# Optimization experiments

Hardware: AMD Instinct MI355X
Metric: run time of the kernel (lower is better)

## Reference

```python
import jax, jax.numpy as jnp
import numpy as np

# Mamba2 defaults with d_model=512, headdim=2*d_model (=> nheads=1)
D_MODEL = 512
D_INNER = 2 * D_MODEL          # expand=2
D_STATE = 128
NHEADS = 1                     # d_inner // headdim = 1
HEADDIM = D_INNER              # headdim = 2*hidden_dim
D_CONV = 4
NG = 1                         # ngroups
EPS = 1e-5


def setup_inputs() -> dict:
    key = jax.random.key(0)
    ks = jax.random.split(key, 8)
    B, L = 4, 2048
    d_in_proj = 2 * D_INNER + 2 * NG * D_STATE + NHEADS   # 2305
    conv_ch = D_INNER + 2 * NG * D_STATE                  # 1280
    x = jax.random.normal(ks[0], (B, L, D_MODEL), jnp.float32)
    rnn_state = jax.random.normal(ks[1], (B, D_MODEL), jnp.float32)
    W_in = jax.random.normal(ks[2], (d_in_proj, D_MODEL), jnp.float32) * (D_MODEL ** -0.5)
    conv_w = jax.random.normal(ks[3], (conv_ch, 1, D_CONV), jnp.float32) * (D_CONV ** -0.5)
    conv_b = jnp.zeros((conv_ch,), jnp.float32)
    # dt_bias = inv_softplus(dt) with dt ~ U(1e-3, 0.1), as in Mamba2 init
    dt = jax.random.uniform(ks[4], (NHEADS,), jnp.float32, 1e-3, 0.1)
    dt_bias = jnp.log(jnp.expm1(dt))
    A_log = jnp.log(jax.random.uniform(ks[5], (NHEADS,), jnp.float32, 1.0, 16.0))
    Dp = jnp.ones((NHEADS,), jnp.float32)
    norm_w = jnp.ones((D_INNER,), jnp.float32)
    W_out = jax.random.normal(ks[6], (D_MODEL, D_INNER), jnp.float32) * (D_INNER ** -0.5)
    return dict(x=x, rnn_state=rnn_state, W_in=W_in, conv_w=conv_w, conv_b=conv_b,
                dt_bias=dt_bias, A_log=A_log, Dp=Dp, norm_w=norm_w, W_out=W_out)


def _mamba2(x, W_in, conv_w, conv_b, dt_bias, A_log, Dp, norm_w, W_out):
    B, L, _ = x.shape
    zxbcdt = jnp.einsum('bld,ed->ble', x, W_in)           # (B,L,2305)
    z, xBC, dt = jnp.split(zxbcdt, [D_INNER, 2 * D_INNER + 2 * NG * D_STATE], axis=-1)
    # causal depthwise conv1d over channels (B,C,L), then silu
    xBC = xBC.transpose(0, 2, 1)
    xBC = jax.lax.conv_general_dilated(
        xBC, conv_w, window_strides=(1,), padding=[(D_CONV - 1, 0)],
        feature_group_count=xBC.shape[1], dimension_numbers=('NCH', 'OIH', 'NCH'))
    xBC = jax.nn.silu(xBC + conv_b[None, :, None]).transpose(0, 2, 1)
    xs, Bm, Cm = jnp.split(xBC, [D_INNER, D_INNER + NG * D_STATE], axis=-1)
    xs = xs.reshape(B, L, NHEADS, HEADDIM)
    dt = jax.nn.softplus(dt + dt_bias)                    # (B,L,H)
    A = -jnp.exp(A_log)                                   # (H,)
    dA = jnp.exp(dt * A)                                  # (B,L,H)

    # selective state-space scan: h_t = dA_t*h_{t-1} + dt_t * x_t (x) B_t ; y_t = h_t @ C_t
    def step(state, inp):
        x_t, dt_t, dA_t, B_t, C_t = inp
        state = dA_t[:, :, None, None] * state \
            + (dt_t[:, :, None] * x_t)[..., None] * B_t[:, None, None, :]
        y_t = jnp.einsum('bhpn,bn->bhp', state, C_t)
        return state, y_t

    init = jnp.zeros((B, NHEADS, HEADDIM, D_STATE), x.dtype)
    inputs = (xs.transpose(1, 0, 2, 3), dt.transpose(1, 0, 2), dA.transpose(1, 0, 2),
              Bm.transpose(1, 0, 2), Cm.transpose(1, 0, 2))
    _, ys = jax.lax.scan(step, init, inputs)              # (L,B,H,P)
    y = ys.transpose(1, 0, 2, 3) + Dp[None, None, :, None] * xs
    y = y.reshape(B, L, D_INNER)
    # gated RMSNorm (gate first, norm_before_gate=False)
    y = y * jax.nn.silu(z)
    y = y * jax.lax.rsqrt(jnp.mean(y * y, axis=-1, keepdims=True) + EPS) * norm_w
    return jnp.einsum('bld,od->blo', y, W_out)


def reference(x, rnn_state, W_in, conv_w, conv_b, dt_bias, A_log, Dp, norm_w, W_out):
    out = _mamba2(x, W_in, conv_w, conv_b, dt_bias, A_log, Dp, norm_w, W_out)
    return (out, rnn_state)
```

## Files before the change

### kernel.cpp

```cpp
#include <hip/hip_runtime.h>
#include <cstdint>
#include <cstddef>


typedef __bf16 bf16_t;
typedef __bf16 bf16x8 __attribute__((ext_vector_type(8)));
typedef __bf16 bf16x4 __attribute__((ext_vector_type(4)));
typedef __bf16 bf16x2 __attribute__((ext_vector_type(2)));
typedef float  f32x4  __attribute__((ext_vector_type(4)));

#define BATCH   4
#define SEQLEN  2048
#define MROWS   8192
#define DMODEL  512
#define DINNER  1024
#define DSTATE  128
#define NZX     2304
#define NCONV   1280
#define CHUNK   128
#define NCHUNK  16
#define NBC     64

__device__ __forceinline__ float siluf(float x) { return x / (1.f + __expf(-x)); }

__device__ __forceinline__ void load_lds16(const bf16_t* g, bf16_t* l)
{
    __builtin_amdgcn_global_load_lds(
        (const __attribute__((address_space(1))) void*)g,
        (__attribute__((address_space(3))) void*)l,
        16, 0, 0);
}

template <typename OutT>
__device__ __forceinline__ void gemm64_body(
    unsigned char* smem,
    const bf16_t* __restrict__ A, const bf16_t* __restrict__ B,
    OutT* __restrict__ C, int Ntot, int K, int lda, int ldb, int bn, int bm)
{
    bf16_t* As = (bf16_t*)smem;
    bf16_t* Bs = (bf16_t*)(smem + 8192);

    const int tid  = threadIdx.x;
    const int wave = tid >> 6, lane = tid & 63;
    const int lr = lane & 15, q = lane >> 4;
    const int wm = (wave & 1) * 32, wn = (wave >> 1) * 64;

    f32x4 acc[2][4];
    #pragma unroll
    for (int i = 0; i < 2; ++i)
        #pragma unroll
        for (int j = 0; j < 4; ++j)
            acc[i][j] = (f32x4){0.f, 0.f, 0.f, 0.f};

    const int row_a0 = bm * 64, row_b0 = bn * 128;
    const int srow = tid >> 3;
    const int gsw  = (((tid & 7) ^ (srow & 7))) * 8;
    const int lsl  = (tid & 7) * 8;

    for (int kt = 0; kt < K; kt += 64) {
        #pragma unroll
        for (int i = 0; i < 2; ++i) {
            int row = srow + i * 32;
            load_lds16(&A[(size_t)(row_a0 + row) * lda + kt + gsw], &As[row * 64 + lsl]);
        }
        #pragma unroll
        for (int i = 0; i < 4; ++i) {
            int row = srow + i * 32;
            load_lds16(&B[(size_t)(row_b0 + row) * ldb + kt + gsw], &Bs[row * 64 + lsl]);
        }
        __syncthreads();
        #pragma unroll
        for (int k0 = 0; k0 < 64; k0 += 32) {
            bf16x8 af[2], bfr[4];
            #pragma unroll
            for (int mi = 0; mi < 2; ++mi) {
                int r = wm + mi * 16 + lr, kc = (k0 >> 3) + q;
                af[mi] = *reinterpret_cast<const bf16x8*>(
                    &As[r * 64 + ((kc ^ (r & 7)) << 3)]);
            }
            #pragma unroll
            for (int ni = 0; ni < 4; ++ni) {
                int r = wn + ni * 16 + lr, kc = (k0 >> 3) + q;
                bfr[ni] = *reinterpret_cast<const bf16x8*>(
                    &Bs[r * 64 + ((kc ^ (r & 7)) << 3)]);
            }
            #pragma unroll
            for (int mi = 0; mi < 2; ++mi)
                #pragma unroll
                for (int ni = 0; ni < 4; ++ni)
                    acc[mi][ni] = __builtin_amdgcn_mfma_f32_16x16x32_bf16(
                        af[mi], bfr[ni], acc[mi][ni], 0, 0, 0);
        }
        __syncthreads();
    }

    #pragma unroll
    for (int mi = 0; mi < 2; ++mi)
        #pragma unroll
        for (int ni = 0; ni < 4; ++ni)
            #pragma unroll
            for (int ri = 0; ri < 4; ++ri) {
                int row = row_a0 + wm + mi * 16 + q * 4 + ri;
                int col = row_b0 + wn + ni * 16 + lr;
                C[(size_t)row * Ntot + col] = (OutT)acc[mi][ni][ri];
            }
}

__device__ __forceinline__ void cumsum_body(
    const float* __restrict__ dtv, const float* __restrict__ A_log,
    float* __restrict__ sarr, float* __restrict__ Pv,
    float* __restrict__ EdTv, float* __restrict__ chp, int bc)
{
    __shared__ float w0sum, stot;
    int j = threadIdx.x;
    bool active = j < CHUNK;
    int lane = j & 63;
    int r = bc * CHUNK + j;
    float A = -expf(A_log[0]);
    float dt = active ? dtv[r] : 0.f;
    float s = dt;
    #pragma unroll
    for (int m = 1; m <= 32; m <<= 1) {
        float o = __shfl_up(s, m);
        if (lane >= m) s += o;
    }
    if (j == 63) w0sum = s;
    __syncthreads();
    if (j >= 64 && active) s += w0sum;
    if (j == 127) stot = s;
    __syncthreads();
    if (active) {
        float sT = stot;
        sarr[r] = s;
        Pv[r]   = expf(A * s);
        EdTv[r] = expf(A * (sT - s)) * dt;
        if (j == 127) chp[bc] = expf(A * sT);
    }
}

__global__ __launch_bounds__(256) void gemm1_kernel(
    const bf16_t* __restrict__ xb, const bf16_t* __restrict__ winb,
    bf16_t* __restrict__ zx, const float* __restrict__ dtv,
    const float* __restrict__ A_log, float* __restrict__ sarr,
    float* __restrict__ Pv, float* __restrict__ EdTv, float* __restrict__ chp)
{
    __shared__ __align__(16) unsigned char smem[24576];
    int linear = blockIdx.x;
    if (linear < (NZX / 128) * (MROWS / 64)) {
        int xcd = linear & 7, j = linear >> 3;
        int bm = xcd * 16 + (j & 15);
        int bn = j >> 4;
        gemm64_body<bf16_t>(smem, xb, winb, zx, NZX, DMODEL, DMODEL, DMODEL, bn, bm);
    } else {
        cumsum_body(dtv, A_log, sarr, Pv, EdTv, chp, linear - 2304);
    }
}

__global__ __launch_bounds__(256) void gemm2_kernel(
    const bf16_t* __restrict__ yb, const bf16_t* __restrict__ woutb,
    float* __restrict__ out)
{
    __shared__ __align__(16) unsigned char smem[24576];
    int id  = blockIdx.x;
    int xcd = id & 7, j = id >> 3;
    int bm  = xcd * 16 + (j & 15);
    int bn  = j >> 4;
    gemm64_body<float>(smem, yb, woutb, out, DMODEL, DINNER, DINNER, DINNER, bn, bm);
}

__device__ __forceinline__ void mbuild_body(
    unsigned char* smem,
    const float* __restrict__ sarr, const float* __restrict__ dtv,
    const float* __restrict__ Pv, const float* __restrict__ A_log,
    const bf16_t* __restrict__ xbc, bf16_t* __restrict__ Mx, int bc)
{
    bf16_t* Cs  = (bf16_t*)smem;
    bf16_t* Bs2 = (bf16_t*)(smem + 32768);
    float* sj = (float*)(smem + 65536);
    float* dj = (float*)(smem + 65536 + 512);
    float* pj = (float*)(smem + 65536 + 1024);

    int tid = threadIdx.x;
    if (tid < CHUNK) {
        sj[tid] = sarr[bc * CHUNK + tid];
        dj[tid] = dtv[bc * CHUNK + tid];
        pj[tid] = Pv[bc * CHUNK + tid];
    }
    int rowbase = bc * 128;
    int srow = tid >> 4;
    int gsw  = (((tid & 15) ^ (srow & 7))) * 8;
    int lsl  = (tid & 15) * 8;
    #pragma unroll
    for (int i = 0; i < 8; ++i) {
        int row = srow + i * 16;
        load_lds16(&xbc[(size_t)(rowbase + row) * NCONV + 1152 + gsw], &Cs[row * 128 + lsl]);
        load_lds16(&xbc[(size_t)(rowbase + row) * NCONV + 1024 + gsw], &Bs2[row * 128 + lsl]);
    }
    __syncthreads();

    const int wave = tid >> 6, lane = tid & 63;
    const int lr = lane & 15, q = lane >> 4;
    const int wm = (wave & 1) * 64, wn = (wave >> 1) * 64;

    f32x4 acc[4][4];
    #pragma unroll
    for (int i = 0; i < 4; ++i)
        #pragma unroll
        for (int j = 0; j < 4; ++j)
            acc[i][j] = (f32x4){0.f, 0.f, 0.f, 0.f};

    #pragma unroll
    for (int k0 = 0; k0 < 128; k0 += 32) {
        bf16x8 af[4], bfr[4];
        #pragma unroll
        for (int mi = 0; mi < 4; ++mi) {
            int r = wm + mi * 16 + lr, kc = (k0 >> 3) + q;
            af[mi] = *reinterpret_cast<const bf16x8*>(
                &Cs[r * 128 + ((kc ^ (r & 7)) << 3)]);
        }
        #pragma unroll
        for (int ni = 0; ni < 4; ++ni) {
            int r = wn + ni * 16 + lr, kc = (k0 >> 3) + q;
            bfr[ni] = *reinterpret_cast<const bf16x8*>(
                &Bs2[r * 128 + ((kc ^ (r & 7)) << 3)]);
        }
        #pragma unroll
        for (int mi = 0; mi < 4; ++mi)
            #pragma unroll
            for (int ni = 0; ni < 4; ++ni)
                acc[mi][ni] = __builtin_amdgcn_mfma_f32_16x16x32_bf16(
                    af[mi], bfr[ni], acc[mi][ni], 0, 0, 0);
    }

    float A = -expf(A_log[0]);
    bf16_t* MxB = Mx + (size_t)bc * 32768;
    #pragma unroll
    for (int mi = 0; mi < 4; ++mi)
        #pragma unroll
        for (int ni = 0; ni < 4; ++ni)
            #pragma unroll
            for (int ri = 0; ri < 4; ++ri) {
                int row = wm + mi * 16 + q * 4 + ri;
                int col = wn + ni * 16 + lr;
                float val = 0.f;
                if (col <= row)
                    val = acc[mi][ni][ri] * expf(A * (sj[row] - sj[col])) * dj[col];
                MxB[(size_t)row * 256 + col] = (bf16_t)val;
            }

    int rr = tid >> 1, cb2 = (tid & 1) * 64;
    float Pi = pj[rr];
    #pragma unroll
    for (int m0 = 0; m0 < 64; m0 += 8) {
        int kc = (cb2 + m0) >> 3;
        bf16x8 cv = *reinterpret_cast<const bf16x8*>(
            &Cs[rr * 128 + ((kc ^ (rr & 7)) << 3)]);
        bf16x8 o;
        #pragma unroll
        for (int m = 0; m < 8; ++m) o[m] = (bf16_t)((float)cv[m] * Pi);
        *reinterpret_cast<bf16x8*>(&MxB[(size_t)rr * 256 + 128 + cb2 + m0]) = o;
    }
}

__global__ __launch_bounds__(256) void gemmA_mbuild_kernel(
    const bf16_t* __restrict__ Xt, const bf16_t* __restrict__ Bwt,
    bf16_t* __restrict__ cstate,
    const float* __restrict__ sarr, const float* __restrict__ dtv,
    const float* __restrict__ Pv, const float* __restrict__ A_log,
    const bf16_t* __restrict__ xbc, bf16_t* __restrict__ Mx)
{
    __shared__ __align__(16) unsigned char smem[67072];
    int id = blockIdx.x;
    if (id < 1024) {
        int bc = id & 63, bm = id >> 6;
        gemm64_body<bf16_t>(smem,
            Xt + (size_t)bc * 131072, Bwt + (size_t)bc * 16384,
            cstate + (size_t)bc * 131072,
            DSTATE, CHUNK, CHUNK, CHUNK, 0, bm);
    } else {
        mbuild_body(smem, sarr, dtv, Pv, A_log, xbc, Mx, id - 1024);
    }
}

__global__ __launch_bounds__(256) void gemm_y_kernel(
    const bf16_t* __restrict__ Mx, const bf16_t* __restrict__ Xt,
    const bf16_t* __restrict__ Stb, bf16_t* __restrict__ yf)
{
    __shared__ __align__(16) bf16_t As[64 * 64];
    __shared__ __align__(16) bf16_t Bs[128 * 64];

    int id = blockIdx.x;
    int bc = id & 63;
    int t  = id >> 6;
    int half = t & 1, bn = t >> 1;

    const bf16_t* Ab = Mx  + (size_t)bc * 32768 + (size_t)half * 64 * 256;
    const bf16_t* Xb = Xt  + (size_t)bc * 131072 + (size_t)bn * 128 * 128;
    const bf16_t* Sb = Stb + (size_t)bc * 131072 + (size_t)bn * 128 * 128;
    bf16_t* Cb = yf + (size_t)bc * 131072 + (size_t)half * 64 * 1024;

    const int tid  = threadIdx.x;
    const int wave = tid >> 6, lane = tid & 63;
    const int lr = lane & 15, q = lane >> 4;
    const int wm = (wave & 1) * 32, wn = (wave >> 1) * 64;

    f32x4 acc[2][4];
    #pragma unroll
    for (int i = 0; i < 2; ++i)
        #pragma unroll
        for (int j = 0; j < 4; ++j)
            acc[i][j] = (f32x4){0.f, 0.f, 0.f, 0.f};

    const int srow = tid >> 3;
    const int gsw  = (((tid & 7) ^ (srow & 7))) * 8;
    const int lsl  = (tid & 7) * 8;

    for (int kt = 0; kt < 256; kt += 64) {
        const bf16_t* bsrc = (kt < 128) ? (Xb + kt) : (Sb + (kt - 128));
        #pragma unroll
        for (int i = 0; i < 2; ++i) {
            int row = srow + i * 32;
            load_lds16(&Ab[(size_t)row * 256 + kt + gsw], &As[row * 64 + lsl]);
        }
        #pragma unroll
        for (int i = 0; i < 4; ++i) {
            int row = srow + i * 32;
            load_lds16(&bsrc[(size_t)row * 128 + gsw], &Bs[row * 64 + lsl]);
        }
        __syncthreads();
        #pragma unroll
        for (int k0 = 0; k0 < 64; k0 += 32) {
            bf16x8 af[2], bfr[4];
            #pragma unroll
            for (int mi = 0; mi < 2; ++mi) {
                int r = wm + mi * 16 + lr, kc = (k0 >> 3) + q;
                af[mi] = *reinterpret_cast<const bf16x8*>(
                    &As[r * 64 + ((kc ^ (r & 7)) << 3)]);
            }
            #pragma unroll
            for (int ni = 0; ni < 4; ++ni) {
                int r = wn + ni * 16 + lr, kc = (k0 >> 3) + q;
                bfr[ni] = *reinterpret_cast<const bf16x8*>(
                    &Bs[r * 64 + ((kc ^ (r & 7)) << 3)]);
            }
            #pragma unroll
            for (int mi = 0; mi < 2; ++mi)
                #pragma unroll
                for (int ni = 0; ni < 4; ++ni)
                    acc[mi][ni] = __builtin_amdgcn_mfma_f32_16x16x32_bf16(
                        af[mi], bfr[ni], acc[mi][ni], 0, 0, 0);
        }
        __syncthreads();
    }

    #pragma unroll
    for (int mi = 0; mi < 2; ++mi)
        #pragma unroll
        for (int ni = 0; ni < 4; ++ni)
            #pragma unroll
            for (int ri = 0; ri < 4; ++ri) {
                int row = wm + mi * 16 + q * 4 + ri;
                int col = bn * 128 + wn + ni * 16 + lr;
                Cb[(size_t)row * 1024 + col] = (bf16_t)acc[mi][ni][ri];
            }
}

__global__ __launch_bounds__(256) void dtcast_kernel(
    const float* __restrict__ x, const float* __restrict__ W_in,
    const float* __restrict__ dt_bias, const float* __restrict__ W_out,
    float* __restrict__ dtv, bf16_t* __restrict__ xb,
    bf16_t* __restrict__ winb, bf16_t* __restrict__ woutb)
{
    int bid = blockIdx.x;
    if (bid < MROWS / 4) {
        int wave = threadIdx.x >> 6, lane = threadIdx.x & 63;
        int r = bid * 4 + wave;
        const float* xr = x + (size_t)r * DMODEL + lane * 8;
        const float* wr = W_in + (size_t)NZX * DMODEL + lane * 8;
        float4 a0 = *reinterpret_cast<const float4*>(xr);
        float4 a1 = *reinterpret_cast<const float4*>(xr + 4);
        float4 b0 = *reinterpret_cast<const float4*>(wr);
        float4 b1 = *reinterpret_cast<const float4*>(wr + 4);

        bf16x8 xo;
        xo[0] = (bf16_t)a0.x; xo[1] = (bf16_t)a0.y; xo[2] = (bf16_t)a0.z; xo[3] = (bf16_t)a0.w;
        xo[4] = (bf16_t)a1.x; xo[5] = (bf16_t)a1.y; xo[6] = (bf16_t)a1.z; xo[7] = (bf16_t)a1.w;
        *reinterpret_cast<bf16x8*>(xb + (size_t)r * DMODEL + lane * 8) = xo;

        float s = a0.x * b0.x + a0.y * b0.y + a0.z * b0.z + a0.w * b0.w
                + a1.x * b1.x + a1.y * b1.y + a1.z * b1.z + a1.w * b1.w;
        #pragma unroll
        for (int m = 32; m >= 1; m >>= 1) s += __shfl_xor(s, m);
        if (lane == 0) {
            float t  = s + dt_bias[0];
            dtv[r] = (t > 20.f) ? t : log1pf(expf(t));
        }
        return;
    }
    int i = (bid - MROWS / 4) * 256 + threadIdx.x;
    const int n4a = 2305 * DMODEL / 4, n4b = DMODEL * DINNER / 4;
    const float* src; bf16_t* dst; int j;
    if (i < n4a)            { src = W_in;  dst = winb;  j = i; }
    else if (i < n4a + n4b) { src = W_out; dst = woutb; j = i - n4a; }
    else return;
    float4 v = reinterpret_cast<const float4*>(src)[j];
    bf16x4 o;
    o[0] = (bf16_t)v.x; o[1] = (bf16_t)v.y; o[2] = (bf16_t)v.z; o[3] = (bf16_t)v.w;
    reinterpret_cast<bf16x4*>(dst)[j] = o;
}

__global__ __launch_bounds__(256) void conv_tr_kernel(
    const bf16_t* __restrict__ zx, const float* __restrict__ cw,
    const float* __restrict__ cb, const float* __restrict__ EdTv,
    bf16_t* __restrict__ xbc, bf16_t* __restrict__ Xt, bf16_t* __restrict__ Bwt)
{
    constexpr int TS = 66;
    __shared__ bf16_t tile[128 * TS];
    __shared__ float cwS[64 * 4];
    __shared__ float cbS[64];

    int id  = blockIdx.x;
    int xcd = id & 7;
    int k   = id >> 3;
    int bc  = xcd * 8 + (k & 7);
    int rest = k >> 3;
    int cg   = rest >> 1;
    int half = rest & 1;
    int c0   = cg * 128 + half * 64;
    int tid  = threadIdx.x;

    if (tid < 64) {
        float4 w = *reinterpret_cast<const float4*>(cw + (size_t)(c0 + tid) * 4);
        *reinterpret_cast<float4*>(&cwS[tid * 4]) = w;
        cbS[tid] = cb[c0 + tid];
    }
    __syncthreads();

    int lrow = tid >> 3;
    int lc8  = (tid & 7) * 8;
    int g0 = bc * 128;

    #pragma unroll
    for (int pass = 0; pass < 4; ++pass) {
        int row = pass * 32 + lrow;
        int g = g0 + row;
        int l = g & (SEQLEN - 1);
        float acc[8];
        #pragma unroll
        for (int m = 0; m < 8; ++m) acc[m] = cbS[lc8 + m];
        #pragma unroll
        for (int kk = 0; kk < 4; ++kk) {
            if (l + kk >= 3) {
                bf16x8 v = *reinterpret_cast<const bf16x8*>(
                    zx + (size_t)(g + kk - 3) * NZX + DINNER + c0 + lc8);
                #pragma unroll
                for (int m = 0; m < 8; ++m)
                    acc[m] += cwS[(lc8 + m) * 4 + kk] * (float)v[m];
            }
        }
        bf16x8 o;
        #pragma unroll
        for (int m = 0; m < 8; ++m) o[m] = (bf16_t)siluf(acc[m]);
        *reinterpret_cast<bf16x8*>(xbc + (size_t)g * NCONV + c0 + lc8) = o;
        if (cg < 9) {
            #pragma unroll
            for (int jj = 0; jj < 4; ++jj) {
                bf16x2 p; p[0] = o[jj * 2]; p[1] = o[jj * 2 + 1];
                *reinterpret_cast<bf16x2*>(&tile[row * TS + lc8 + jj * 2]) = p;
            }
        }
    }
    if (cg == 9) return;
    __syncthreads();

    const bool isB = (cg == 8);
    int jo = (tid >> 4) * 8;
    int i  = tid & 15;
    float sc[8];
    #pragma unroll
    for (int m = 0; m < 8; ++m)
        sc[m] = isB ? EdTv[bc * 128 + jo + m] : 1.f;

    #pragma unroll
    for (int pass = 0; pass < 4; ++pass) {
        int oc = pass * 16 + i;
        bf16x8 o;
        #pragma unroll
        for (int m = 0; m < 8; ++m)
            o[m] = (bf16_t)((float)tile[(jo + m) * TS + oc] * sc[m]);
        bf16_t* dst = isB
            ? (Bwt + (size_t)bc * 16384 + (size_t)(c0 - 1024 + oc) * 128 + jo)
            : (Xt + (size_t)bc * 131072 + (size_t)(c0 + oc) * 128 + jo);
        *reinterpret_cast<bf16x8*>(dst) = o;
    }
}

__global__ __launch_bounds__(256) void scan_combine_kernel(
    const bf16_t* __restrict__ cstate, const float* __restrict__ chp,
    bf16_t* __restrict__ Stb)
{
    __shared__ float chS[NCHUNK];
    int idx = blockIdx.x * 256 + threadIdx.x;
    int b   = idx >> 17;
    int np  = idx & 131071;
    if (threadIdx.x < NCHUNK) chS[threadIdx.x] = chp[b * NCHUNK + threadIdx.x];
    __syncthreads();

    const bf16_t* src = cstate + ((size_t)b << 21) + np;
    bf16_t*       dst = Stb    + ((size_t)b << 21) + np;
    float t[NCHUNK];
    #pragma unroll
    for (int c = 0; c < NCHUNK; ++c) t[c] = (float)src[(size_t)c << 17];
    float v = 0.f;
    #pragma unroll
    for (int c = 0; c < NCHUNK; ++c) {
        dst[(size_t)c << 17] = (bf16_t)v;
        v = chS[c] * v + t[c];
    }
}

__global__ __launch_bounds__(256) void gate_norm_kernel(
    const bf16_t* __restrict__ yf, const bf16_t* __restrict__ zx,
    const bf16_t* __restrict__ xbc, const float* __restrict__ Dp,
    const float* __restrict__ norm_w, bf16_t* __restrict__ yb,
    const float* __restrict__ rnn, float* __restrict__ outTail)
{
    int blk = blockIdx.x, tid = threadIdx.x;
    if (blk >= MROWS / 4) {
        int i = (blk - MROWS / 4) * 256 + tid;
        if (i < BATCH * DMODEL) outTail[i] = rnn[i];
        return;
    }
    int wave = tid >> 6, lane = tid & 63;
    int r = blk * 4 + wave;
    int p0 = lane * 8, p1 = 512 + lane * 8;
    float D0 = Dp[0];

    bf16x8 y0 = *reinterpret_cast<const bf16x8*>(yf + (size_t)r * DINNER + p0);
    bf16x8 y1 = *reinterpret_cast<const bf16x8*>(yf + (size_t)r * DINNER + p1);
    bf16x8 z0 = *reinterpret_cast<const bf16x8*>(zx + (size_t)r * NZX + p0);
    bf16x8 z1 = *reinterpret_cast<const bf16x8*>(zx + (size_t)r * NZX + p1);
    bf16x8 x0 = *reinterpret_cast<const bf16x8*>(xbc + (size_t)r * NCONV + p0);
    bf16x8 x1 = *reinterpret_cast<const bf16x8*>(xbc + (size_t)r * NCONV + p1);

    float g[16];
    #pragma unroll
    for (int m = 0; m < 8; ++m) {
        g[m]     = ((float)y0[m] + D0 * (float)x0[m]) * siluf((float)z0[m]);
        g[8 + m] = ((float)y1[m] + D0 * (float)x1[m]) * siluf((float)z1[m]);
    }
    float ss = 0.f;
    #pragma unroll
    for (int m = 0; m < 16; ++m) ss += g[m] * g[m];
    #pragma unroll
    for (int m = 32; m >= 1; m >>= 1) ss += __shfl_xor(ss, m);
    float scale = rsqrtf(ss * (1.f / 1024.f) + 1e-5f);

    const float* nw = norm_w;
    float4 w0a = *reinterpret_cast<const float4*>(nw + p0);
    float4 w0b = *reinterpret_cast<const float4*>(nw + p0 + 4);
    float4 w1a = *reinterpret_cast<const float4*>(nw + p1);
    float4 w1b = *reinterpret_cast<const float4*>(nw + p1 + 4);
    float w[16] = {w0a.x, w0a.y, w0a.z, w0a.w, w0b.x, w0b.y, w0b.z, w0b.w,
                   w1a.x, w1a.y, w1a.z, w1a.w, w1b.x, w1b.y, w1b.z, w1b.w};
    bf16x8 o0, o1;
    #pragma unroll
    for (int m = 0; m < 8; ++m) {
        o0[m] = (bf16_t)(g[m] * scale * w[m]);
        o1[m] = (bf16_t)(g[8 + m] * scale * w[8 + m]);
    }
    *reinterpret_cast<bf16x8*>(yb + (size_t)r * DINNER + p0) = o0;
    *reinterpret_cast<bf16x8*>(yb + (size_t)r * DINNER + p1) = o1;
}

extern "C" void kernel_launch(void* const* d_in, const int* in_sizes, int n_in,
                              void* d_out, int out_size, void* d_ws, size_t ws_size,
                              hipStream_t stream)
{
    const float* x        = (const float*)d_in[0];
    const float* rnn      = (const float*)d_in[1];
    const float* W_in     = (const float*)d_in[2];
    const float* conv_w   = (const float*)d_in[3];
    const float* conv_b   = (const float*)d_in[4];
    const float* dt_bias  = (const float*)d_in[5];
    const float* A_log    = (const float*)d_in[6];
    const float* Dp       = (const float*)d_in[7];
    const float* norm_w   = (const float*)d_in[8];
    const float* W_out    = (const float*)d_in[9];
    float* out = (float*)d_out;

    char* ws = (char*)d_ws;
    bf16_t* xb     = (bf16_t*)(ws + 0);
    bf16_t* Mx     = (bf16_t*)(ws + 4194304);
    bf16_t* winb   = (bf16_t*)(ws + 8388608);
    bf16_t* woutb  = (bf16_t*)(ws + 10748928);
    bf16_t* zx     = (bf16_t*)(ws + 11797504);
    float*  dtv    = (float*) (ws + 49546240);
    float*  sarr   = (float*) (ws + 49579008);
    float*  Pv     = (float*) (ws + 49611776);
    float*  EdTv   = (float*) (ws + 49644544);
    float*  chp    = (float*) (ws + 49677312);
    bf16_t* xbcb   = (bf16_t*)(ws + 49677568);
    bf16_t* Xt     = (bf16_t*)(ws + 70649088);
    bf16_t* Bwt    = (bf16_t*)(ws + 87426304);
    bf16_t* cstate = (bf16_t*)(ws + 89523456);
    bf16_t* yf     = (bf16_t*)(ws + 89523456);
    bf16_t* Stb    = (bf16_t*)(ws + 106300672);
    bf16_t* yb     = (bf16_t*)(ws + 123077888);

    {
        const int n4a = 2305 * DMODEL / 4, n4b = DMODEL * DINNER / 4;
        int grid = MROWS / 4 + (n4a + n4b + 255) / 256;
        dtcast_kernel<<<grid, 256, 0, stream>>>(
            x, W_in, dt_bias, W_out, dtv, xb, winb, woutb);
    }

    gemm1_kernel<<<2304 + NBC, 256, 0, stream>>>(
        xb, winb, zx, dtv, A_log, sarr, Pv, EdTv, chp);

    conv_tr_kernel<<<1280, 256, 0, stream>>>(
        zx, conv_w, conv_b, EdTv, xbcb, Xt, Bwt);

    gemmA_mbuild_kernel<<<1088, 256, 0, stream>>>(
        Xt, Bwt, cstate, sarr, dtv, Pv, A_log, xbcb, Mx);

    scan_combine_kernel<<<BATCH * 131072 / 256, 256, 0, stream>>>(cstate, chp, Stb);

    gemm_y_kernel<<<1024, 256, 0, stream>>>(Mx, Xt, Stb, yf);

    gate_norm_kernel<<<MROWS / 4 + 8, 256, 0, stream>>>(
        yf, zx, xbcb, Dp, norm_w, yb, rnn, out + (size_t)MROWS * DMODEL);

    gemm2_kernel<<<512, 256, 0, stream>>>(yb, woutb, out);
}
```

Measured before the change: 193.6 us.

## Shrink GEMM tiles to 64x64, split mbuild into quarters, fuse it with scan

Adds a 64x64-tile GEMM body and uses it for the chunk-state GEMM, the output projection and the y GEMM, doubling their grid sizes. The intra-chunk M-matrix build is split into four 64x64 sub-blocks with less shared memory, then moved from the gemmA kernel into the scan-combine kernel. The aim is more blocks, higher occupancy and better load balance across CUs. In exchange each block reuses less data, so global and LDS traffic per FLOP rises, and the wave count per launch goes up.

```diff
diff --git a/kernel.cpp b/kernel.cpp
--- a/kernel.cpp
+++ b/kernel.cpp
@@ -106,6 +106,77 @@
             }
 }
 
+template <typename OutT>
+__device__ __forceinline__ void gemm6464_body(
+    unsigned char* smem,
+    const bf16_t* __restrict__ A, const bf16_t* __restrict__ B,
+    OutT* __restrict__ C, int Ntot, int K, int lda, int ldb, int bn, int bm)
+{
+    bf16_t* As = (bf16_t*)smem;
+    bf16_t* Bs = (bf16_t*)(smem + 8192);
+
+    const int tid  = threadIdx.x;
+    const int wave = tid >> 6, lane = tid & 63;
+    const int lr = lane & 15, q = lane >> 4;
+    const int wm = (wave & 1) * 32, wn = (wave >> 1) * 32;
+
+    f32x4 acc[2][2];
+    #pragma unroll
+    for (int i = 0; i < 2; ++i)
+        #pragma unroll
+        for (int j = 0; j < 2; ++j)
+            acc[i][j] = (f32x4){0.f, 0.f, 0.f, 0.f};
+
+    const int row_a0 = bm * 64, row_b0 = bn * 64;
+    const int srow = tid >> 3;
+    const int gsw  = (((tid & 7) ^ (srow & 7))) * 8;
+    const int lsl  = (tid & 7) * 8;
+
+    for (int kt = 0; kt < K; kt += 64) {
+        #pragma unroll
+        for (int i = 0; i < 2; ++i) {
+            int row = srow + i * 32;
+            load_lds16(&A[(size_t)(row_a0 + row) * lda + kt + gsw], &As[row * 64 + lsl]);
+            load_lds16(&B[(size_t)(row_b0 + row) * ldb + kt + gsw], &Bs[row * 64 + lsl]);
+        }
+        __syncthreads();
+        #pragma unroll
+        for (int k0 = 0; k0 < 64; k0 += 32) {
+            bf16x8 af[2], bfr[2];
+            #pragma unroll
+            for (int mi = 0; mi < 2; ++mi) {
+                int r = wm + mi * 16 + lr, kc = (k0 >> 3) + q;
+                af[mi] = *reinterpret_cast<const bf16x8*>(
+                    &As[r * 64 + ((kc ^ (r & 7)) << 3)]);
+            }
+            #pragma unroll
+            for (int ni = 0; ni < 2; ++ni) {
+                int r = wn + ni * 16 + lr, kc = (k0 >> 3) + q;
+                bfr[ni] = *reinterpret_cast<const bf16x8*>(
+                    &Bs[r * 64 + ((kc ^ (r & 7)) << 3)]);
+            }
+            #pragma unroll
+            for (int mi = 0; mi < 2; ++mi)
+                #pragma unroll
+                for (int ni = 0; ni < 2; ++ni)
+                    acc[mi][ni] = __builtin_amdgcn_mfma_f32_16x16x32_bf16(
+                        af[mi], bfr[ni], acc[mi][ni], 0, 0, 0);
+        }
+        __syncthreads();
+    }
+
+    #pragma unroll
+    for (int mi = 0; mi < 2; ++mi)
+        #pragma unroll
+        for (int ni = 0; ni < 2; ++ni)
+            #pragma unroll
+            for (int ri = 0; ri < 4; ++ri) {
+                int row = row_a0 + wm + mi * 16 + q * 4 + ri;
+                int col = row_b0 + wn + ni * 16 + lr;
+                C[(size_t)row * Ntot + col] = (OutT)acc[mi][ni][ri];
+            }
+}
+
 __device__ __forceinline__ void cumsum_body(
     const float* __restrict__ dtv, const float* __restrict__ A_log,
     float* __restrict__ sarr, float* __restrict__ Pv,
@@ -160,25 +231,44 @@
     const bf16_t* __restrict__ yb, const bf16_t* __restrict__ woutb,
     float* __restrict__ out)
 {
-    __shared__ __align__(16) unsigned char smem[24576];
+    __shared__ __align__(16) unsigned char smem[16384];
     int id  = blockIdx.x;
     int xcd = id & 7, j = id >> 3;
     int bm  = xcd * 16 + (j & 15);
     int bn  = j >> 4;
-    gemm64_body<float>(smem, yb, woutb, out, DMODEL, DINNER, DINNER, DINNER, bn, bm);
-}
-
-__device__ __forceinline__ void mbuild_body(
+    gemm6464_body<float>(smem, yb, woutb, out, DMODEL, DINNER, DINNER, DINNER, bn, bm);
+}
+
+__global__ __launch_bounds__(256) void gemmA_kernel(
+    const bf16_t* __restrict__ Xt, const bf16_t* __restrict__ Bwt,
+    bf16_t* __restrict__ cstate)
+{
+    __shared__ __align__(16) unsigned char smem[16384];
+    int id = blockIdx.x;
+    int bc = id & 63;
+    int t  = id >> 6;
+    int bm = t >> 1, bn = t & 1;
+    gemm6464_body<bf16_t>(smem,
+        Xt + (size_t)bc * 131072, Bwt + (size_t)bc * 16384,
+        cstate + (size_t)bc * 131072,
+        DSTATE, CHUNK, CHUNK, CHUNK, bn, bm);
+}
+
+__device__ __forceinline__ void mbuild64_body(
     unsigned char* smem,
     const float* __restrict__ sarr, const float* __restrict__ dtv,
     const float* __restrict__ Pv, const float* __restrict__ A_log,
-    const bf16_t* __restrict__ xbc, bf16_t* __restrict__ Mx, int bc)
-{
+    const bf16_t* __restrict__ xbc, bf16_t* __restrict__ Mx, int sub)
+{
+    int bc = sub & 63;
+    int t  = sub >> 6;
+    int bm = t >> 1, bn = t & 1;
+
     bf16_t* Cs  = (bf16_t*)smem;
-    bf16_t* Bs2 = (bf16_t*)(smem + 32768);
-    float* sj = (float*)(smem + 65536);
-    float* dj = (float*)(smem + 65536 + 512);
-    float* pj = (float*)(smem + 65536 + 1024);
+    bf16_t* Bs2 = (bf16_t*)(smem + 16384);
+    float* sj = (float*)(smem + 32768);
+    float* dj = sj + 128;
+    float* pj = dj + 128;
 
     int tid = threadIdx.x;
     if (tid < CHUNK) {
@@ -191,43 +281,45 @@
     int gsw  = (((tid & 15) ^ (srow & 7))) * 8;
     int lsl  = (tid & 15) * 8;
     #pragma unroll
-    for (int i = 0; i < 8; ++i) {
+    for (int i = 0; i < 4; ++i) {
         int row = srow + i * 16;
-        load_lds16(&xbc[(size_t)(rowbase + row) * NCONV + 1152 + gsw], &Cs[row * 128 + lsl]);
-        load_lds16(&xbc[(size_t)(rowbase + row) * NCONV + 1024 + gsw], &Bs2[row * 128 + lsl]);
+        load_lds16(&xbc[(size_t)(rowbase + bm * 64 + row) * NCONV + 1152 + gsw],
+                   &Cs[row * 128 + lsl]);
+        load_lds16(&xbc[(size_t)(rowbase + bn * 64 + row) * NCONV + 1024 + gsw],
+                   &Bs2[row * 128 + lsl]);
     }
     __syncthreads();
 
     const int wave = tid >> 6, lane = tid & 63;
     const int lr = lane & 15, q = lane >> 4;
-    const int wm = (wave & 1) * 64, wn = (wave >> 1) * 64;
-
-    f32x4 acc[4][4];
-    #pragma unroll
-    for (int i = 0; i < 4; ++i)
-        #pragma unroll
-        for (int j = 0; j < 4; ++j)
+    const int wm = (wave & 1) * 32, wn = (wave >> 1) * 32;
+
+    f32x4 acc[2][2];
+    #pragma unroll
+    for (int i = 0; i < 2; ++i)
+        #pragma unroll
+        for (int j = 0; j < 2; ++j)
             acc[i][j] = (f32x4){0.f, 0.f, 0.f, 0.f};
 
     #pragma unroll
     for (int k0 = 0; k0 < 128; k0 += 32) {
-        bf16x8 af[4], bfr[4];
-        #pragma unroll
-        for (int mi = 0; mi < 4; ++mi) {
+        bf16x8 af[2], bfr[2];
+        #pragma unroll
+        for (int mi = 0; mi < 2; ++mi) {
             int r = wm + mi * 16 + lr, kc = (k0 >> 3) + q;
             af[mi] = *reinterpret_cast<const bf16x8*>(
                 &Cs[r * 128 + ((kc ^ (r & 7)) << 3)]);
         }
         #pragma unroll
-        for (int ni = 0; ni < 4; ++ni) {
+        for (int ni = 0; ni < 2; ++ni) {
             int r = wn + ni * 16 + lr, kc = (k0 >> 3) + q;
             bfr[ni] = *reinterpret_cast<const bf16x8*>(
                 &Bs2[r * 128 + ((kc ^ (r & 7)) << 3)]);
         }
         #pragma unroll
-        for (int mi = 0; mi < 4; ++mi)
-            #pragma unroll
-            for (int ni = 0; ni < 4; ++ni)
+        for (int mi = 0; mi < 2; ++mi)
+            #pragma unroll
+            for (int ni = 0; ni < 2; ++ni)
                 acc[mi][ni] = __builtin_amdgcn_mfma_f32_16x16x32_bf16(
                     af[mi], bfr[ni], acc[mi][ni], 0, 0, 0);
     }
@@ -235,50 +327,75 @@
     float A = -expf(A_log[0]);
     bf16_t* MxB = Mx + (size_t)bc * 32768;
     #pragma unroll
-    for (int mi = 0; mi < 4; ++mi)
-        #pragma unroll
-        for (int ni = 0; ni < 4; ++ni)
+    for (int mi = 0; mi < 2; ++mi)
+        #pragma unroll
+        for (int ni = 0; ni < 2; ++ni)
             #pragma unroll
             for (int ri = 0; ri < 4; ++ri) {
-                int row = wm + mi * 16 + q * 4 + ri;
-                int col = wn + ni * 16 + lr;
+                int row = bm * 64 + wm + mi * 16 + q * 4 + ri;
+                int col = bn * 64 + wn + ni * 16 + lr;
                 float val = 0.f;
                 if (col <= row)
                     val = acc[mi][ni][ri] * expf(A * (sj[row] - sj[col])) * dj[col];
                 MxB[(size_t)row * 256 + col] = (bf16_t)val;
             }
 
-    int rr = tid >> 1, cb2 = (tid & 1) * 64;
-    float Pi = pj[rr];
-    #pragma unroll
-    for (int m0 = 0; m0 < 64; m0 += 8) {
-        int kc = (cb2 + m0) >> 3;
-        bf16x8 cv = *reinterpret_cast<const bf16x8*>(
-            &Cs[rr * 128 + ((kc ^ (rr & 7)) << 3)]);
-        bf16x8 o;
-        #pragma unroll
-        for (int m = 0; m < 8; ++m) o[m] = (bf16_t)((float)cv[m] * Pi);
-        *reinterpret_cast<bf16x8*>(&MxB[(size_t)rr * 256 + 128 + cb2 + m0]) = o;
-    }
-}
-
-__global__ __launch_bounds__(256) void gemmA_mbuild_kernel(
-    const bf16_t* __restrict__ Xt, const bf16_t* __restrict__ Bwt,
-    bf16_t* __restrict__ cstate,
+    if (bn == 0) {
+        int rl = tid >> 2;
+        int cb2 = (tid & 3) * 32;
+        float Pi = pj[bm * 64 + rl];
+        #pragma unroll
+        for (int m0 = 0; m0 < 32; m0 += 8) {
+            int kc = (cb2 + m0) >> 3;
+            bf16x8 cv = *reinterpret_cast<const bf16x8*>(
+                &Cs[rl * 128 + ((kc ^ (rl & 7)) << 3)]);
+            bf16x8 o;
+            #pragma unroll
+            for (int m = 0; m < 8; ++m) o[m] = (bf16_t)((float)cv[m] * Pi);
+            *reinterpret_cast<bf16x8*>(
+                &MxB[(size_t)(bm * 64 + rl) * 256 + 128 + cb2 + m0]) = o;
+        }
+    }
+}
+
+__device__ __forceinline__ void scan_body(
+    unsigned char* smem,
+    const bf16_t* __restrict__ cstate, const float* __restrict__ chp,
+    bf16_t* __restrict__ Stb, int blk)
+{
+    float* chS = (float*)smem;
+    int idx = blk * 256 + threadIdx.x;
+    int b   = idx >> 17;
+    int np  = idx & 131071;
+    if (threadIdx.x < NCHUNK) chS[threadIdx.x] = chp[b * NCHUNK + threadIdx.x];
+    __syncthreads();
+
+    const bf16_t* src = cstate + ((size_t)b << 21) + np;
+    bf16_t*       dst = Stb    + ((size_t)b << 21) + np;
+    float t[NCHUNK];
+    #pragma unroll
+    for (int c = 0; c < NCHUNK; ++c) t[c] = (float)src[(size_t)c << 17];
+    float v = 0.f;
+    #pragma unroll
+    for (int c = 0; c < NCHUNK; ++c) {
+        dst[(size_t)c << 17] = (bf16_t)v;
+        v = chS[c] * v + t[c];
+    }
+}
+
+__global__ __launch_bounds__(256) void scan_mbuild_kernel(
+    const bf16_t* __restrict__ cstate, const float* __restrict__ chp,
+    bf16_t* __restrict__ Stb,
     const float* __restrict__ sarr, const float* __restrict__ dtv,
     const float* __restrict__ Pv, const float* __restrict__ A_log,
     const bf16_t* __restrict__ xbc, bf16_t* __restrict__ Mx)
 {
-    __shared__ __align__(16) unsigned char smem[67072];
+    __shared__ __align__(16) unsigned char smem[34304];
     int id = blockIdx.x;
-    if (id < 1024) {
-        int bc = id & 63, bm = id >> 6;
-        gemm64_body<bf16_t>(smem,
-            Xt + (size_t)bc * 131072, Bwt + (size_t)bc * 16384,
-            cstate + (size_t)bc * 131072,
-            DSTATE, CHUNK, CHUNK, CHUNK, 0, bm);
+    if (id < 256) {
+        mbuild64_body(smem, sarr, dtv, Pv, A_log, xbc, Mx, id);
     } else {
-        mbuild_body(smem, sarr, dtv, Pv, A_log, xbc, Mx, id - 1024);
+        scan_body(smem, cstate, chp, Stb, id - 256);
     }
 }
 
@@ -287,7 +404,7 @@
     const bf16_t* __restrict__ Stb, bf16_t* __restrict__ yf)
 {
     __shared__ __align__(16) bf16_t As[64 * 64];
-    __shared__ __align__(16) bf16_t Bs[128 * 64];
+    __shared__ __align__(16) bf16_t Bs[64 * 64];
 
     int id = blockIdx.x;
     int bc = id & 63;
@@ -295,20 +412,20 @@
     int half = t & 1, bn = t >> 1;
 
     const bf16_t* Ab = Mx  + (size_t)bc * 32768 + (size_t)half * 64 * 256;
-    const bf16_t* Xb = Xt  + (size_t)bc * 131072 + (size_t)bn * 128 * 128;
-    const bf16_t* Sb = Stb + (size_t)bc * 131072 + (size_t)bn * 128 * 128;
+    const bf16_t* Xb = Xt  + (size_t)bc * 131072 + (size_t)bn * 64 * 128;
+    const bf16_t* Sb = Stb + (size_t)bc * 131072 + (size_t)bn * 64 * 128;
     bf16_t* Cb = yf + (size_t)bc * 131072 + (size_t)half * 64 * 1024;
 
     const int tid  = threadIdx.x;
     const int wave = tid >> 6, lane = tid & 63;
     const int lr = lane & 15, q = lane >> 4;
-    const int wm = (wave & 1) * 32, wn = (wave >> 1) * 64;
-
-    f32x4 acc[2][4];
+    const int wm = (wave & 1) * 32, wn = (wave >> 1) * 32;
+
+    f32x4 acc[2][2];
     #pragma unroll
     for (int i = 0; i < 2; ++i)
         #pragma unroll
-        for (int j = 0; j < 4; ++j)
+        for (int j = 0; j < 2; ++j)
             acc[i][j] = (f32x4){0.f, 0.f, 0.f, 0.f};
 
     const int srow = tid >> 3;
@@ -321,16 +438,12 @@
         for (int i = 0; i < 2; ++i) {
             int row = srow + i * 32;
             load_lds16(&Ab[(size_t)row * 256 + kt + gsw], &As[row * 64 + lsl]);
-        }
-        #pragma unroll
-        for (int i = 0; i < 4; ++i) {
-            int row = srow + i * 32;
             load_lds16(&bsrc[(size_t)row * 128 + gsw], &Bs[row * 64 + lsl]);
         }
         __syncthreads();
         #pragma unroll
         for (int k0 = 0; k0 < 64; k0 += 32) {
-            bf16x8 af[2], bfr[4];
+            bf16x8 af[2], bfr[2];
             #pragma unroll
             for (int mi = 0; mi < 2; ++mi) {
                 int r = wm + mi * 16 + lr, kc = (k0 >> 3) + q;
@@ -338,7 +451,7 @@
                     &As[r * 64 + ((kc ^ (r & 7)) << 3)]);
             }
             #pragma unroll
-            for (int ni = 0; ni < 4; ++ni) {
+            for (int ni = 0; ni < 2; ++ni) {
                 int r = wn + ni * 16 + lr, kc = (k0 >> 3) + q;
                 bfr[ni] = *reinterpret_cast<const bf16x8*>(
                     &Bs[r * 64 + ((kc ^ (r & 7)) << 3)]);
@@ -346,7 +459,7 @@
             #pragma unroll
             for (int mi = 0; mi < 2; ++mi)
                 #pragma unroll
-                for (int ni = 0; ni < 4; ++ni)
+                for (int ni = 0; ni < 2; ++ni)
                     acc[mi][ni] = __builtin_amdgcn_mfma_f32_16x16x32_bf16(
                         af[mi], bfr[ni], acc[mi][ni], 0, 0, 0);
         }
@@ -356,11 +469,11 @@
     #pragma unroll
     for (int mi = 0; mi < 2; ++mi)
         #pragma unroll
-        for (int ni = 0; ni < 4; ++ni)
+        for (int ni = 0; ni < 2; ++ni)
             #pragma unroll
             for (int ri = 0; ri < 4; ++ri) {
                 int row = wm + mi * 16 + q * 4 + ri;
-                int col = bn * 128 + wn + ni * 16 + lr;
+                int col = bn * 64 + wn + ni * 16 + lr;
                 Cb[(size_t)row * 1024 + col] = (bf16_t)acc[mi][ni][ri];
             }
 }
@@ -492,30 +605,6 @@
             ? (Bwt + (size_t)bc * 16384 + (size_t)(c0 - 1024 + oc) * 128 + jo)
             : (Xt + (size_t)bc * 131072 + (size_t)(c0 + oc) * 128 + jo);
         *reinterpret_cast<bf16x8*>(dst) = o;
-    }
-}
-
-__global__ __launch_bounds__(256) void scan_combine_kernel(
-    const bf16_t* __restrict__ cstate, const float* __restrict__ chp,
-    bf16_t* __restrict__ Stb)
-{
-    __shared__ float chS[NCHUNK];
-    int idx = blockIdx.x * 256 + threadIdx.x;
-    int b   = idx >> 17;
-    int np  = idx & 131071;
-    if (threadIdx.x < NCHUNK) chS[threadIdx.x] = chp[b * NCHUNK + threadIdx.x];
-    __syncthreads();
-
-    const bf16_t* src = cstate + ((size_t)b << 21) + np;
-    bf16_t*       dst = Stb    + ((size_t)b << 21) + np;
-    float t[NCHUNK];
-    #pragma unroll
-    for (int c = 0; c < NCHUNK; ++c) t[c] = (float)src[(size_t)c << 17];
-    float v = 0.f;
-    #pragma unroll
-    for (int c = 0; c < NCHUNK; ++c) {
-        dst[(size_t)c << 17] = (bf16_t)v;
-        v = chS[c] * v + t[c];
     }
 }
 
@@ -621,15 +710,15 @@
     conv_tr_kernel<<<1280, 256, 0, stream>>>(
         zx, conv_w, conv_b, EdTv, xbcb, Xt, Bwt);
 
-    gemmA_mbuild_kernel<<<1088, 256, 0, stream>>>(
-        Xt, Bwt, cstate, sarr, dtv, Pv, A_log, xbcb, Mx);
-
-    scan_combine_kernel<<<BATCH * 131072 / 256, 256, 0, stream>>>(cstate, chp, Stb);
-
-    gemm_y_kernel<<<1024, 256, 0, stream>>>(Mx, Xt, Stb, yf);
+    gemmA_kernel<<<2048, 256, 0, stream>>>(Xt, Bwt, cstate);
+
+    scan_mbuild_kernel<<<256 + BATCH * 131072 / 256, 256, 0, stream>>>(
+        cstate, chp, Stb, sarr, dtv, Pv, A_log, xbcb, Mx);
+
+    gemm_y_kernel<<<2048, 256, 0, stream>>>(Mx, Xt, Stb, yf);
 
     gate_norm_kernel<<<MROWS / 4 + 8, 256, 0, stream>>>(
         yf, zx, xbcb, Dp, norm_w, yb, rnn, out + (size_t)MROWS * DMODEL);
 
-    gemm2_kernel<<<512, 256, 0, stream>>>(yb, woutb, out);
-}
+    gemm2_kernel<<<1024, 256, 0, stream>>>(yb, woutb, out);
+}
```

Result: no change. 190.2 us (-1.8%).
